# Optimization experiments

Measured on AMD Instinct MI355X. Metric: run time of the kernel, lower is better.

Reference implementation:

```python
import jax, jax.numpy as jnp
import numpy as np

EPS = 1e-12  # F.normalize eps

def setup_inputs() -> dict:
    key = jax.random.key(0)
    k1, k2, k3, k4 = jax.random.split(key, 4)
    B, N, IN, OUT = 8, 2048, 128, 128
    x = jax.random.normal(k1, (B, N, IN), dtype=jnp.float32)
    edge_weight = jax.random.uniform(k2, (B, N, N), dtype=jnp.float32)
    # Linear params (torch nn.Linear: y = x @ W.T + b)
    bound = 1.0 / np.sqrt(IN)
    W = jax.random.uniform(k3, (OUT, IN), minval=-bound, maxval=bound, dtype=jnp.float32)
    b = jax.random.uniform(k4, (OUT,), minval=-bound, maxval=bound, dtype=jnp.float32)
    return {"x": x, "edge_weight": edge_weight, "W": W, "b": b}

def reference(x, edge_weight, W, b):
    # Linear: [B,N,IN] -> [B,N,OUT]
    h = jnp.einsum('bni,oi->bno', x, W) + b
    # L2 normalize along feature dim (F.normalize, eps-clamped denominator)
    norm = jnp.sqrt(jnp.sum(h * h, axis=-1, keepdims=True))
    hn = h / jnp.maximum(norm, EPS)
    # pairwise cosine similarity [B,N,N]
    cos = jnp.einsum('bij,bkj->bik', hn, hn)
    gated = edge_weight * cos
    # weighted aggregation [B,N,OUT]
    out = jnp.einsum('bpq,bqc->bpc', gated, h)
    # is_last=False, dropout p=0.0 -> ReLU only
    return jax.nn.relu(out)
```

## Files before the change

### kernel.cpp

```cpp
#include <hip/hip_runtime.h>

#define NB 8
#define NN 2048
#define ND 128

typedef float f32x4 __attribute__((ext_vector_type(4)));
typedef __bf16 bf16x8 __attribute__((ext_vector_type(8)));
typedef unsigned short u16x4 __attribute__((ext_vector_type(4)));

__device__ __forceinline__ unsigned short f2bf(float f) {
  unsigned u = __builtin_bit_cast(unsigned, f);
  u = (u + 0x7FFFu + ((u >> 16) & 1u)) >> 16;
  return (unsigned short)u;
}

__device__ __forceinline__ void stage16(const void* g, void* l) {
  __builtin_amdgcn_global_load_lds(
      (const __attribute__((address_space(1))) unsigned int*)g,
      (__attribute__((address_space(3))) unsigned int*)l, 16, 0, 0);
}

__global__ __launch_bounds__(512, 2) void k_linear(
    const float* __restrict__ x, const float* __restrict__ W,
    const float* __restrict__ bias,
    unsigned short* __restrict__ hn, unsigned short* __restrict__ hT) {
  __shared__ __align__(16) float xs[128][68];
  __shared__ __align__(16) float wt[128][128];
  const int tid = threadIdx.x;
  const int rbase = blockIdx.x * 64;
  const int b = rbase >> 11;
  const int nb = rbase & (NN - 1);

#pragma unroll
  for (int j = 0; j < 4; ++j) {
    int f = tid + j * 512;
    int row = f >> 5;
    int kc = (f & 31) << 2;
    f32x4 v = *reinterpret_cast<const f32x4*>(&x[(size_t)(rbase + row) * ND + kc]);
#pragma unroll
    for (int i2 = 0; i2 < 4; ++i2) {
      int k = kc + i2;
      xs[k][row ^ (k & 28)] = v[i2];
    }
  }
#pragma unroll
  for (int j = 0; j < 8; ++j) {
    int f = tid + j * 512;
    int o = f >> 5;
    int i0 = (f & 31) << 2;
    f32x4 v = *reinterpret_cast<const f32x4*>(&W[(size_t)o * ND + i0]);
#pragma unroll
    for (int i2 = 0; i2 < 4; ++i2) {
      int k = i0 + i2;
      wt[k][o ^ (k & 28)] = v[i2];
    }
  }
  __syncthreads();

  const int tc = tid & 31;
  const int tr = tid >> 5;

  float acc[4][4];
#pragma unroll
  for (int r = 0; r < 4; ++r)
#pragma unroll
    for (int c = 0; c < 4; ++c) acc[r][c] = 0.f;

#pragma unroll 4
  for (int k = 0; k < 128; ++k) {
    const int sw = k & 28;
    f32x4 xv = *reinterpret_cast<const f32x4*>(&xs[k][(tr * 4) ^ sw]);
    f32x4 wv = *reinterpret_cast<const f32x4*>(&wt[k][(tc * 4) ^ sw]);
#pragma unroll
    for (int r = 0; r < 4; ++r)
#pragma unroll
      for (int c = 0; c < 4; ++c) acc[r][c] += xv[r] * wv[c];
  }

  f32x4 bv = *reinterpret_cast<const f32x4*>(&bias[tc * 4]);
#pragma unroll
  for (int r = 0; r < 4; ++r)
#pragma unroll
    for (int c = 0; c < 4; ++c) acc[r][c] += bv[c];

  float inv[4];
#pragma unroll
  for (int r = 0; r < 4; ++r) {
    float s = acc[r][0] * acc[r][0] + acc[r][1] * acc[r][1] +
              acc[r][2] * acc[r][2] + acc[r][3] * acc[r][3];
#pragma unroll
    for (int d = 1; d < 32; d <<= 1) s += __shfl_xor(s, d, 32);
    inv[r] = 1.f / fmaxf(sqrtf(s), 1e-12f);
  }

#pragma unroll
  for (int r = 0; r < 4; ++r) {
    u16x4 hv;
#pragma unroll
    for (int c = 0; c < 4; ++c) hv[c] = f2bf(acc[r][c] * inv[r]);
    *reinterpret_cast<u16x4*>(&hn[(size_t)(rbase + tr * 4 + r) * ND + tc * 4]) = hv;
  }
#pragma unroll
  for (int c = 0; c < 4; ++c) {
    u16x4 tv;
#pragma unroll
    for (int r = 0; r < 4; ++r) tv[r] = f2bf(acc[r][c]);
    *reinterpret_cast<u16x4*>(
        &hT[((size_t)b * ND + tc * 4 + c) * NN + nb + tr * 4]) = tv;
  }
}

__global__ __launch_bounds__(512) void k_fused(
    const float* __restrict__ edge,
    const unsigned short* __restrict__ hn,
    const unsigned short* __restrict__ hT,
    float* __restrict__ part) {
  __shared__ __align__(16) unsigned short Klds[2][32 * 128];
  __shared__ __align__(16) unsigned short Vlds[2][32 * 128];
  __shared__ __align__(16) float Elds[2][256 * 32];
  __shared__ __align__(16) unsigned short p_lds[8][2][16][32];

  const int tid = threadIdx.x;
  const int w = tid >> 6;
  const int l = tid & 63;
  const int m = l & 15;
  const int g = l >> 4;

  const int bid = blockIdx.x;
  const int b = bid & 7;
  const int qt = (bid >> 3) & 7;
  const int kh = bid >> 6;

  const int q00 = qt * 256;
  const int q0 = q00 + w * 16;
  const unsigned short* hnb = hn + (size_t)b * NN * ND;
  const unsigned short* hTb = hT + (size_t)b * ND * NN;
  const float* eb = edge + (size_t)b * NN * NN;

  bf16x8 bq[2][4];
#pragma unroll
  for (int f = 0; f < 2; ++f) {
    const unsigned short* qp = hnb + (size_t)(q0 + f * 128 + m) * ND + g * 8;
#pragma unroll
    for (int kst = 0; kst < 4; ++kst)
      bq[f][kst] = *reinterpret_cast<const bf16x8*>(qp + kst * 32);
  }

  f32x4 acc_o[2][8];
#pragma unroll
  for (int f = 0; f < 2; ++f)
#pragma unroll
    for (int i = 0; i < 8; ++i) acc_o[f][i] = (f32x4){0.f, 0.f, 0.f, 0.f};

  auto STAGE = [&](int kt, int buf) {
    const int kb = kh * 512 + kt * 32;
    {
      int r = tid >> 4, c = tid & 15;
      int lg = c ^ (r & 15);
      stage16(hnb + (size_t)(kb + r) * ND + lg * 8,
              (char*)&Klds[buf][0] + (size_t)(w * 64) * 16);
    }
    {
      int fr = tid >> 4, c = tid & 15;
      int lg = c ^ (fr & 15);
      int ft = fr * 4 + (lg >> 2);
      stage16(hTb + (size_t)ft * NN + kb + (lg & 3) * 8,
              (char*)&Vlds[buf][0] + (size_t)(w * 64) * 16);
    }
#pragma unroll
    for (int i = 0; i < 4; ++i) {
      int ch = tid + i * 512;
      int r2 = ch >> 3, c = ch & 7;
      int lg = c ^ (r2 & 7);
      stage16(eb + (size_t)(q00 + r2) * NN + kb + lg * 4,
              (char*)&Elds[buf][0] + (size_t)(w * 64 + i * 512) * 16);
    }
  };

  auto TILE = [&](int t, int A) {
    if (t < 15) {
      STAGE(t + 1, A ^ 1);
      asm volatile("s_waitcnt vmcnt(6)" ::: "memory");
    } else {
      asm volatile("s_waitcnt vmcnt(0)" ::: "memory");
    }
    __builtin_amdgcn_s_barrier();

    const unsigned short* Ka = &Klds[A][0];
    const unsigned short* Va = &Vlds[A][0];
    const float* Ea = &Elds[A][0];

    f32x4 st[2][2];
#pragma unroll
    for (int f = 0; f < 2; ++f)
#pragma unroll
      for (int ct = 0; ct < 2; ++ct) st[f][ct] = (f32x4){0.f, 0.f, 0.f, 0.f};
#pragma unroll
    for (int kst = 0; kst < 4; ++kst) {
      bf16x8 ak[2];
#pragma unroll
      for (int ct = 0; ct < 2; ++ct) {
        const int r = ct * 16 + m;
        const int ph = (kst * 4 + g) ^ m;
        ak[ct] = *reinterpret_cast<const bf16x8*>(&Ka[r * 128 + ph * 8]);
      }
#pragma unroll
      for (int f = 0; f < 2; ++f)
#pragma unroll
        for (int ct = 0; ct < 2; ++ct)
          st[f][ct] = __builtin_amdgcn_mfma_f32_16x16x32_bf16(ak[ct], bq[f][kst],
                                                              st[f][ct], 0, 0, 0);
    }

#pragma unroll
    for (int f = 0; f < 2; ++f)
#pragma unroll
      for (int ct = 0; ct < 2; ++ct) {
        const int ro = f * 128 + w * 16 + m;
        const int pe = (ct * 4 + g) ^ (m & 7);
        f32x4 ev = *reinterpret_cast<const f32x4*>(&Ea[ro * 32 + pe * 4]);
        u16x4 pv;
#pragma unroll
        for (int r = 0; r < 4; ++r) pv[r] = f2bf(ev[r] * st[f][ct][r]);
        const int ls = ct * 2 + (g >> 1);
        const int ps = ls ^ (m >> 2);
        *reinterpret_cast<u16x4*>(&p_lds[w][f][m][ps * 8 + (g & 1) * 4]) = pv;
      }

    {
      bf16x8 bv[8];
#pragma unroll
      for (int ct2 = 0; ct2 < 8; ++ct2) {
        const int c2 = ct2 * 16 + m;
        const int fr = c2 >> 2;
        const int lg = (c2 & 3) * 4 + g;
        const int ph = lg ^ (fr & 15);
        bv[ct2] = *reinterpret_cast<const bf16x8*>(&Va[fr * 128 + ph * 8]);
      }
      const int psa = g ^ (m >> 2);
#pragma unroll
      for (int f = 0; f < 2; ++f) {
        bf16x8 ap = *reinterpret_cast<const bf16x8*>(&p_lds[w][f][m][psa * 8]);
#pragma unroll
        for (int ct2 = 0; ct2 < 8; ++ct2)
          acc_o[f][ct2] = __builtin_amdgcn_mfma_f32_16x16x32_bf16(
              ap, bv[ct2], acc_o[f][ct2], 0, 0, 0);
      }
    }

    __builtin_amdgcn_s_barrier();
  };

  STAGE(0, 0);
#pragma unroll 1
  for (int t2 = 0; t2 < 8; ++t2) {
    TILE(2 * t2, 0);
    TILE(2 * t2 + 1, 1);
  }

  float* pb = part + (size_t)kh * (NB * NN * ND);
#pragma unroll
  for (int f = 0; f < 2; ++f) {
    float* pf = pb + ((size_t)b * NN + q0 + f * 128) * ND;
#pragma unroll
    for (int ct2 = 0; ct2 < 8; ++ct2)
#pragma unroll
      for (int r = 0; r < 4; ++r)
        pf[(size_t)(g * 4 + r) * ND + ct2 * 16 + m] = acc_o[f][ct2][r];
  }
}

__global__ __launch_bounds__(256) void k_merge(const float* __restrict__ part,
                                               float* __restrict__ out, int n4) {
  int i = blockIdx.x * 256 + threadIdx.x;
  if (i >= n4) return;
  const f32x4* p = reinterpret_cast<const f32x4*>(part);
  const size_t s = (size_t)NB * NN * ND / 4;
  f32x4 v = p[i] + p[i + s] + p[i + 2 * s] + p[i + 3 * s];
#pragma unroll
  for (int j = 0; j < 4; ++j) v[j] = fmaxf(v[j], 0.f);
  reinterpret_cast<f32x4*>(out)[i] = v;
}

extern "C" void kernel_launch(void* const* d_in, const int* in_sizes, int n_in,
                              void* d_out, int out_size, void* d_ws, size_t ws_size,
                              hipStream_t stream) {
  const float* x = (const float*)d_in[0];
  const float* edge = (const float*)d_in[1];
  const float* W = (const float*)d_in[2];
  const float* bias = (const float*)d_in[3];
  float* out = (float*)d_out;

  unsigned short* hn = (unsigned short*)d_ws;
  unsigned short* hT = hn + (size_t)NB * NN * ND;
  float* part = (float*)((char*)d_ws + 2 * (size_t)NB * NN * ND * 2);

  k_linear<<<dim3((NB * NN) / 64), dim3(512), 0, stream>>>(x, W, bias, hn, hT);
  k_fused<<<dim3(256), dim3(512), 0, stream>>>(edge, hn, hT, part);
  const int n4 = out_size / 4;
  k_merge<<<dim3((n4 + 255) / 256), dim3(256), 0, stream>>>(part, out, n4);
}
```

Before: 57.76 us.

## Halve query tile per block, double grid, store partials in bf16

The fused kernel now covers 128 query rows per block instead of 256, so the grid grows from 256 to 512 blocks. Register use and shared-memory use per block drop, which allows higher occupancy (launch bounds 512,4). The four split-K partial outputs are stored as bf16 rather than fp32, which halves partial-buffer write and read traffic in the merge kernel. The cost is that K and V tiles are reloaded twice as often per query row, and summing the partials in bf16 loses precision.

```diff
diff --git a/kernel.cpp b/kernel.cpp
--- a/kernel.cpp
+++ b/kernel.cpp
@@ -7,11 +7,16 @@
 typedef float f32x4 __attribute__((ext_vector_type(4)));
 typedef __bf16 bf16x8 __attribute__((ext_vector_type(8)));
 typedef unsigned short u16x4 __attribute__((ext_vector_type(4)));
+typedef unsigned short u16x8 __attribute__((ext_vector_type(8)));
 
 __device__ __forceinline__ unsigned short f2bf(float f) {
   unsigned u = __builtin_bit_cast(unsigned, f);
   u = (u + 0x7FFFu + ((u >> 16) & 1u)) >> 16;
   return (unsigned short)u;
+}
+__device__ __forceinline__ float bf2f(unsigned short s) {
+  unsigned u = (unsigned)s << 16;
+  return __builtin_bit_cast(float, u);
 }
 
 __device__ __forceinline__ void stage16(const void* g, void* l) {
@@ -110,15 +115,15 @@
   }
 }
 
-__global__ __launch_bounds__(512) void k_fused(
+__global__ __launch_bounds__(512, 4) void k_fused(
     const float* __restrict__ edge,
     const unsigned short* __restrict__ hn,
     const unsigned short* __restrict__ hT,
-    float* __restrict__ part) {
+    unsigned short* __restrict__ part) {
+  __shared__ __align__(16) float Elds[2][128 * 32];
   __shared__ __align__(16) unsigned short Klds[2][32 * 128];
   __shared__ __align__(16) unsigned short Vlds[2][32 * 128];
-  __shared__ __align__(16) float Elds[2][256 * 32];
-  __shared__ __align__(16) unsigned short p_lds[8][2][16][32];
+  __shared__ __align__(16) unsigned short p_lds[8][16][32];
 
   const int tid = threadIdx.x;
   const int w = tid >> 6;
@@ -128,29 +133,26 @@
 
   const int bid = blockIdx.x;
   const int b = bid & 7;
-  const int qt = (bid >> 3) & 7;
-  const int kh = bid >> 6;
-
-  const int q00 = qt * 256;
+  const int qt = (bid >> 3) & 15;
+  const int kh = bid >> 7;
+
+  const int q00 = qt * 128;
   const int q0 = q00 + w * 16;
   const unsigned short* hnb = hn + (size_t)b * NN * ND;
   const unsigned short* hTb = hT + (size_t)b * ND * NN;
   const float* eb = edge + (size_t)b * NN * NN;
 
-  bf16x8 bq[2][4];
-#pragma unroll
-  for (int f = 0; f < 2; ++f) {
-    const unsigned short* qp = hnb + (size_t)(q0 + f * 128 + m) * ND + g * 8;
+  bf16x8 bq[4];
+  {
+    const unsigned short* qp = hnb + (size_t)(q0 + m) * ND + g * 8;
 #pragma unroll
     for (int kst = 0; kst < 4; ++kst)
-      bq[f][kst] = *reinterpret_cast<const bf16x8*>(qp + kst * 32);
-  }
-
-  f32x4 acc_o[2][8];
-#pragma unroll
-  for (int f = 0; f < 2; ++f)
-#pragma unroll
-    for (int i = 0; i < 8; ++i) acc_o[f][i] = (f32x4){0.f, 0.f, 0.f, 0.f};
+      bq[kst] = *reinterpret_cast<const bf16x8*>(qp + kst * 32);
+  }
+
+  f32x4 acc_o[8];
+#pragma unroll
+  for (int i = 0; i < 8; ++i) acc_o[i] = (f32x4){0.f, 0.f, 0.f, 0.f};
 
   auto STAGE = [&](int kt, int buf) {
     const int kb = kh * 512 + kt * 32;
@@ -168,7 +170,7 @@
               (char*)&Vlds[buf][0] + (size_t)(w * 64) * 16);
     }
 #pragma unroll
-    for (int i = 0; i < 4; ++i) {
+    for (int i = 0; i < 2; ++i) {
       int ch = tid + i * 512;
       int r2 = ch >> 3, c = ch & 7;
       int lg = c ^ (r2 & 7);
@@ -180,7 +182,7 @@
   auto TILE = [&](int t, int A) {
     if (t < 15) {
       STAGE(t + 1, A ^ 1);
-      asm volatile("s_waitcnt vmcnt(6)" ::: "memory");
+      asm volatile("s_waitcnt vmcnt(4)" ::: "memory");
     } else {
       asm volatile("s_waitcnt vmcnt(0)" ::: "memory");
     }
@@ -190,11 +192,9 @@
     const unsigned short* Va = &Vlds[A][0];
     const float* Ea = &Elds[A][0];
 
-    f32x4 st[2][2];
-#pragma unroll
-    for (int f = 0; f < 2; ++f)
-#pragma unroll
-      for (int ct = 0; ct < 2; ++ct) st[f][ct] = (f32x4){0.f, 0.f, 0.f, 0.f};
+    f32x4 st[2];
+#pragma unroll
+    for (int ct = 0; ct < 2; ++ct) st[ct] = (f32x4){0.f, 0.f, 0.f, 0.f};
 #pragma unroll
     for (int kst = 0; kst < 4; ++kst) {
       bf16x8 ak[2];
@@ -205,27 +205,22 @@
         ak[ct] = *reinterpret_cast<const bf16x8*>(&Ka[r * 128 + ph * 8]);
       }
 #pragma unroll
-      for (int f = 0; f < 2; ++f)
-#pragma unroll
-        for (int ct = 0; ct < 2; ++ct)
-          st[f][ct] = __builtin_amdgcn_mfma_f32_16x16x32_bf16(ak[ct], bq[f][kst],
-                                                              st[f][ct], 0, 0, 0);
-    }
-
-#pragma unroll
-    for (int f = 0; f < 2; ++f)
-#pragma unroll
-      for (int ct = 0; ct < 2; ++ct) {
-        const int ro = f * 128 + w * 16 + m;
-        const int pe = (ct * 4 + g) ^ (m & 7);
-        f32x4 ev = *reinterpret_cast<const f32x4*>(&Ea[ro * 32 + pe * 4]);
-        u16x4 pv;
-#pragma unroll
-        for (int r = 0; r < 4; ++r) pv[r] = f2bf(ev[r] * st[f][ct][r]);
-        const int ls = ct * 2 + (g >> 1);
-        const int ps = ls ^ (m >> 2);
-        *reinterpret_cast<u16x4*>(&p_lds[w][f][m][ps * 8 + (g & 1) * 4]) = pv;
-      }
+      for (int ct = 0; ct < 2; ++ct)
+        st[ct] = __builtin_amdgcn_mfma_f32_16x16x32_bf16(ak[ct], bq[kst], st[ct], 0, 0, 0);
+    }
+
+#pragma unroll
+    for (int ct = 0; ct < 2; ++ct) {
+      const int ro = w * 16 + m;
+      const int pe = (ct * 4 + g) ^ (m & 7);
+      f32x4 ev = *reinterpret_cast<const f32x4*>(&Ea[ro * 32 + pe * 4]);
+      u16x4 pv;
+#pragma unroll
+      for (int r = 0; r < 4; ++r) pv[r] = f2bf(ev[r] * st[ct][r]);
+      const int ls = ct * 2 + (g >> 1);
+      const int ps = ls ^ (m >> 2);
+      *reinterpret_cast<u16x4*>(&p_lds[w][m][ps * 8 + (g & 1) * 4]) = pv;
+    }
 
     {
       bf16x8 bv[8];
@@ -238,14 +233,10 @@
         bv[ct2] = *reinterpret_cast<const bf16x8*>(&Va[fr * 128 + ph * 8]);
       }
       const int psa = g ^ (m >> 2);
-#pragma unroll
-      for (int f = 0; f < 2; ++f) {
-        bf16x8 ap = *reinterpret_cast<const bf16x8*>(&p_lds[w][f][m][psa * 8]);
-#pragma unroll
-        for (int ct2 = 0; ct2 < 8; ++ct2)
-          acc_o[f][ct2] = __builtin_amdgcn_mfma_f32_16x16x32_bf16(
-              ap, bv[ct2], acc_o[f][ct2], 0, 0, 0);
-      }
+      bf16x8 ap = *reinterpret_cast<const bf16x8*>(&p_lds[w][m][psa * 8]);
+#pragma unroll
+      for (int ct2 = 0; ct2 < 8; ++ct2)
+        acc_o[ct2] = __builtin_amdgcn_mfma_f32_16x16x32_bf16(ap, bv[ct2], acc_o[ct2], 0, 0, 0);
     }
 
     __builtin_amdgcn_s_barrier();
@@ -258,28 +249,37 @@
     TILE(2 * t2 + 1, 1);
   }
 
-  float* pb = part + (size_t)kh * (NB * NN * ND);
-#pragma unroll
-  for (int f = 0; f < 2; ++f) {
-    float* pf = pb + ((size_t)b * NN + q0 + f * 128) * ND;
-#pragma unroll
-    for (int ct2 = 0; ct2 < 8; ++ct2)
-#pragma unroll
-      for (int r = 0; r < 4; ++r)
-        pf[(size_t)(g * 4 + r) * ND + ct2 * 16 + m] = acc_o[f][ct2][r];
-  }
-}
-
-__global__ __launch_bounds__(256) void k_merge(const float* __restrict__ part,
-                                               float* __restrict__ out, int n4) {
+  unsigned short* pf =
+      part + (size_t)kh * (NB * NN * ND) + ((size_t)b * NN + q0) * ND;
+#pragma unroll
+  for (int ct2 = 0; ct2 < 8; ++ct2)
+#pragma unroll
+    for (int r = 0; r < 4; ++r)
+      pf[(size_t)(g * 4 + r) * ND + ct2 * 16 + m] = f2bf(acc_o[ct2][r]);
+}
+
+__global__ __launch_bounds__(256) void k_merge(const unsigned short* __restrict__ part,
+                                               float* __restrict__ out, int n8) {
   int i = blockIdx.x * 256 + threadIdx.x;
-  if (i >= n4) return;
-  const f32x4* p = reinterpret_cast<const f32x4*>(part);
-  const size_t s = (size_t)NB * NN * ND / 4;
-  f32x4 v = p[i] + p[i + s] + p[i + 2 * s] + p[i + 3 * s];
-#pragma unroll
-  for (int j = 0; j < 4; ++j) v[j] = fmaxf(v[j], 0.f);
-  reinterpret_cast<f32x4*>(out)[i] = v;
+  if (i >= n8) return;
+  const size_t s = (size_t)NB * NN * ND;
+  float acc[8];
+#pragma unroll
+  for (int j = 0; j < 8; ++j) acc[j] = 0.f;
+#pragma unroll
+  for (int q = 0; q < 4; ++q) {
+    u16x8 v = *reinterpret_cast<const u16x8*>(&part[q * s + (size_t)i * 8]);
+#pragma unroll
+    for (int j = 0; j < 8; ++j) acc[j] += bf2f(v[j]);
+  }
+  f32x4 o0, o1;
+#pragma unroll
+  for (int j = 0; j < 4; ++j) {
+    o0[j] = fmaxf(acc[j], 0.f);
+    o1[j] = fmaxf(acc[4 + j], 0.f);
+  }
+  *reinterpret_cast<f32x4*>(&out[(size_t)i * 8]) = o0;
+  *reinterpret_cast<f32x4*>(&out[(size_t)i * 8 + 4]) = o1;
 }
 
 extern "C" void kernel_launch(void* const* d_in, const int* in_sizes, int n_in,
@@ -293,10 +293,10 @@
 
   unsigned short* hn = (unsigned short*)d_ws;
   unsigned short* hT = hn + (size_t)NB * NN * ND;
-  float* part = (float*)((char*)d_ws + 2 * (size_t)NB * NN * ND * 2);
+  unsigned short* part = hT + (size_t)NB * NN * ND;
 
   k_linear<<<dim3((NB * NN) / 64), dim3(512), 0, stream>>>(x, W, bias, hn, hT);
-  k_fused<<<dim3(256), dim3(512), 0, stream>>>(edge, hn, hT, part);
-  const int n4 = out_size / 4;
-  k_merge<<<dim3((n4 + 255) / 256), dim3(256), 0, stream>>>(part, out, n4);
-}
+  k_fused<<<dim3(512), dim3(512), 0, stream>>>(edge, hn, hT, part);
+  const int n8 = out_size / 8;
+  k_merge<<<dim3((n8 + 255) / 256), dim3(256), 0, stream>>>(part, out, n8);
+}
```

Result: faster. 52.71 us, median of 3 (-8.7%).
